# Kernel optimization log

Measured on AMD Instinct MI355X. Metric: run time of the kernel, lower is better.

## Reference

```python
import jax, jax.numpy as jnp
import numpy as np

N, E, F_IN, H, D, C = 50000, 800000, 128, 4, 64, 40
HD = H * D
NEG_SLOPE = 0.2


def setup_inputs() -> dict:
    key = jax.random.key(0)
    ks = jax.random.split(key, 16)
    x = jax.random.normal(ks[0], (N, F_IN), dtype=jnp.float32)
    edge_index = jax.random.randint(ks[1], (2, E), 0, N, dtype=jnp.int64)
    def glorot(k, shape):
        fan = shape[0] + shape[-1]
        return jax.random.normal(k, shape, dtype=jnp.float32) * jnp.sqrt(2.0 / fan)
    params = {
        'W1': glorot(ks[2], (F_IN, HD)), 'as1': glorot(ks[3], (H, D)), 'ad1': glorot(ks[4], (H, D)), 'b1': jnp.zeros((HD,), jnp.float32),
        'W2': glorot(ks[5], (HD, HD)),   'as2': glorot(ks[6], (H, D)), 'ad2': glorot(ks[7], (H, D)), 'b2': jnp.zeros((HD,), jnp.float32),
        'W3': glorot(ks[8], (HD, HD)),   'as3': glorot(ks[9], (H, D)), 'ad3': glorot(ks[10], (H, D)), 'b3': jnp.zeros((HD,), jnp.float32),
        'Wl': glorot(ks[11], (HD, C)),   'bl': jnp.zeros((C,), jnp.float32),
    }
    return {'x': x, 'edge_index': edge_index, **params}


def gat_layer(x, src, dst, W, a_src, a_dst, b):
    # x: [N, F] -> h: [N, H, D]
    h = (x @ W).reshape(N, H, D)
    alpha_s = jnp.sum(h * a_src, axis=-1)  # [N, H]
    alpha_d = jnp.sum(h * a_dst, axis=-1)  # [N, H]
    e = alpha_s[src] + alpha_d[dst]        # [E', H]
    e = jnp.where(e > 0, e, NEG_SLOPE * e)  # leaky_relu
    # segment softmax over destination nodes
    m = jax.ops.segment_max(e, dst, num_segments=N)  # [N, H]
    m = jnp.where(jnp.isfinite(m), m, 0.0)
    ex = jnp.exp(e - m[dst])
    s = jax.ops.segment_sum(ex, dst, num_segments=N)  # [N, H]
    att = ex / (s[dst] + 1e-16)                        # [E', H]
    # weighted scatter-aggregate of source features
    out = jax.ops.segment_sum(h[src] * att[:, :, None], dst, num_segments=N)  # [N, H, D]
    return out.reshape(N, HD) + b


def reference(x, edge_index, W1, as1, ad1, b1, W2, as2, ad2, b2, W3, as3, ad3, b3, Wl, bl):
    # PyG GATConv adds self-loops by default
    loops = jnp.arange(N, dtype=edge_index.dtype)
    src = jnp.concatenate([edge_index[0], loops])
    dst = jnp.concatenate([edge_index[1], loops])
    # dropout is identity in eval mode
    h = jax.nn.elu(gat_layer(x, src, dst, W1, as1, ad1, b1))
    h = jax.nn.elu(gat_layer(h, src, dst, W2, as2, ad2, b2))
    h = jax.nn.elu(gat_layer(h, src, dst, W3, as3, ad3, b3))
    logits = h @ Wl + bl
    return jax.nn.log_softmax(logits, axis=1)
```

## Files before the change

kernel.cpp:

```cpp
#include <hip/hip_runtime.h>
#include <math.h>

#define NN 50000
#define NE 800000
#define ET (NE + NN)
#define FIN 128
#define HDIM 256
#define NHEAD 4
#define NCLS 40
#define NEG 0.2f
#define NB_SCAN ((NN + 255) / 256)

typedef short bf16x8 __attribute__((ext_vector_type(8)));
typedef float f32x4 __attribute__((ext_vector_type(4)));

__device__ __forceinline__ unsigned short f2b(float f) {
    unsigned int u = __float_as_uint(f);
    unsigned int r = (u + 0x7fffu + ((u >> 16) & 1u)) >> 16;
    return (unsigned short)r;
}
__device__ __forceinline__ float b2f(unsigned short u) {
    unsigned int x = ((unsigned int)u) << 16;
    return __uint_as_float(x);
}

__global__ void detect_kernel(const int* __restrict__ ei32, int* __restrict__ flag) {
    int lane = threadIdx.x;
    int nz = ei32[1 + 2 * lane] | ei32[129 + 2 * lane];
    unsigned long long b = __ballot(nz != 0);
    if (lane == 0) *flag = (b == 0ull) ? 1 : 0;
}

__device__ __forceinline__ int load_node(const int* ei32, int is64, long long idx) {
    return is64 ? ei32[2 * idx] : ei32[idx];
}

__global__ void deg_kernel(const int* __restrict__ ei32, const int* __restrict__ flag,
                           int* __restrict__ deg) {
    int e = blockIdx.x * blockDim.x + threadIdx.x;
    if (e >= ET) return;
    int is64 = *flag;
    int d = (e < NE) ? load_node(ei32, is64, (long long)NE + e) : (e - NE);
    atomicAdd(&deg[d], 1);
}

__global__ void scan1(const int* __restrict__ deg, int* __restrict__ incl,
                      int* __restrict__ bsum) {
    __shared__ int sm[256];
    int i = blockIdx.x * 256 + threadIdx.x;
    int v = (i < NN) ? deg[i] : 0;
    sm[threadIdx.x] = v;
    __syncthreads();
    for (int o = 1; o < 256; o <<= 1) {
        int add = (threadIdx.x >= o) ? sm[threadIdx.x - o] : 0;
        __syncthreads();
        sm[threadIdx.x] += add;
        __syncthreads();
    }
    if (i < NN) incl[i] = sm[threadIdx.x];
    if (threadIdx.x == 255) bsum[blockIdx.x] = sm[255];
}

__global__ void scan2(int* __restrict__ bsum) {
    __shared__ int sm[256];
    int t = threadIdx.x;
    sm[t] = (t < NB_SCAN) ? bsum[t] : 0;
    __syncthreads();
    if (t == 0) {
        int run = 0;
        for (int b = 0; b < NB_SCAN; b++) { int v = sm[b]; sm[b] = run; run += v; }
    }
    __syncthreads();
    if (t < NB_SCAN) bsum[t] = sm[t];
}

__global__ void scan3(const int* __restrict__ incl, const int* __restrict__ bsum,
                      const int* __restrict__ deg, int* __restrict__ indptr,
                      int* __restrict__ cursor) {
    int i = blockIdx.x * 256 + threadIdx.x;
    if (i < NN) {
        int v = bsum[blockIdx.x] + incl[i];
        indptr[i + 1] = v;
        cursor[i] = v - deg[i];
    }
    if (i == 0) indptr[0] = 0;
}

__global__ void fill_kernel(const int* __restrict__ ei32, const int* __restrict__ flag,
                            int* __restrict__ cursor, int* __restrict__ esrc) {
    int e = blockIdx.x * blockDim.x + threadIdx.x;
    if (e >= ET) return;
    int is64 = *flag;
    int s, d;
    if (e < NE) {
        s = load_node(ei32, is64, (long long)e);
        d = load_node(ei32, is64, (long long)NE + e);
    } else {
        s = d = e - NE;
    }
    int pos = atomicAdd(&cursor[d], 1);
    esrc[pos] = s;
}

__global__ __launch_bounds__(256) void wconv3_kernel(const float* __restrict__ W1,
                                                     const float* __restrict__ W2,
                                                     const float* __restrict__ W3,
                                                     unsigned short* __restrict__ Wt1,
                                                     unsigned short* __restrict__ Wt2,
                                                     unsigned short* __restrict__ Wt3) {
    __shared__ float sm[32][33];
    int z = blockIdx.z;
    const float* W = (z == 0) ? W1 : (z == 1) ? W2 : W3;
    unsigned short* Wt = (z == 0) ? Wt1 : (z == 1) ? Wt2 : Wt3;
    int K = (z == 0) ? FIN : HDIM;
    int k0 = blockIdx.y * 32;
    if (k0 >= K) return;
    int tx = threadIdx.x & 31, ty = threadIdx.x >> 5;
    int n0 = blockIdx.x * 32;
#pragma unroll
    for (int j = 0; j < 4; j++)
        sm[ty + j * 8][tx] = W[(size_t)(k0 + ty + j * 8) * HDIM + n0 + tx];
    __syncthreads();
#pragma unroll
    for (int j = 0; j < 4; j++)
        Wt[(size_t)(n0 + ty + j * 8) * K + k0 + tx] = f2b(sm[tx][ty + j * 8]);
}

__global__ __launch_bounds__(256) void gemm_mfma(const unsigned short* __restrict__ A,
                                                 const float* __restrict__ A32,
                                                 const unsigned short* __restrict__ Bt,
                                                 unsigned short* __restrict__ Cb,
                                                 const float* __restrict__ a_s,
                                                 const float* __restrict__ a_d,
                                                 float* __restrict__ als,
                                                 float* __restrict__ ald,
                                                 int M, int K) {
    __shared__ unsigned short As[128][72];
    __shared__ unsigned short Bs[64][72];
    int bid = blockIdx.x;
    int xcd = bid & 7, g = bid >> 3;
    int cblk = g & 3, rg = g >> 2;
    int rblk = rg * 8 + xcd;
    int r0 = rblk * 128, n0 = cblk * 64;
    if (r0 >= M) return;

    int t = threadIdx.x;
    int lane = t & 63, wid = t >> 6;

    f32x4 acc[2][4];
#pragma unroll
    for (int m = 0; m < 2; m++)
#pragma unroll
        for (int n = 0; n < 4; n++)
            acc[m][n] = (f32x4){0.f, 0.f, 0.f, 0.f};

    int ar = t >> 1, ah = (t & 1) * 32;
    int arow = r0 + ar; if (arow > M - 1) arow = M - 1;
    const unsigned short* ga = A + (size_t)arow * K + ah;
    const float* ga32 = A32 ? (A32 + (size_t)arow * K + ah) : (const float*)0;
    int bn = t >> 2, bq = (t & 3) * 16;
    const unsigned short* gb = Bt + (size_t)(n0 + bn) * K + bq;

    int fr = lane & 15;
    int kf = (lane >> 4) * 8;

    for (int k0 = 0; k0 < K; k0 += 64) {
        if (A32) {
#pragma unroll
            for (int j = 0; j < 4; j++) {
                float4 fa = *(const float4*)(ga32 + k0 + j * 8);
                float4 fb = *(const float4*)(ga32 + k0 + j * 8 + 4);
                union { ushort4 u[2]; uint4 v; } pk;
                pk.u[0].x = f2b(fa.x); pk.u[0].y = f2b(fa.y);
                pk.u[0].z = f2b(fa.z); pk.u[0].w = f2b(fa.w);
                pk.u[1].x = f2b(fb.x); pk.u[1].y = f2b(fb.y);
                pk.u[1].z = f2b(fb.z); pk.u[1].w = f2b(fb.w);
                *(uint4*)&As[ar][ah + j * 8] = pk.v;
            }
        } else {
#pragma unroll
            for (int j = 0; j < 4; j++)
                *(uint4*)&As[ar][ah + j * 8] = *(const uint4*)(ga + k0 + j * 8);
        }
#pragma unroll
        for (int j = 0; j < 2; j++)
            *(uint4*)&Bs[bn][bq + j * 8] = *(const uint4*)(gb + k0 + j * 8);
        __syncthreads();
#pragma unroll
        for (int kk = 0; kk < 64; kk += 32) {
            bf16x8 a[2], b[4];
#pragma unroll
            for (int m = 0; m < 2; m++)
                a[m] = *(const bf16x8*)&As[wid * 32 + m * 16 + fr][kk + kf];
#pragma unroll
            for (int n = 0; n < 4; n++)
                b[n] = *(const bf16x8*)&Bs[n * 16 + fr][kk + kf];
#pragma unroll
            for (int m = 0; m < 2; m++)
#pragma unroll
                for (int n = 0; n < 4; n++)
                    acc[m][n] = __builtin_amdgcn_mfma_f32_16x16x32_bf16(a[m], b[n], acc[m][n], 0, 0, 0);
        }
        __syncthreads();
    }

    int rbase = r0 + wid * 32 + (lane >> 4) * 4;
    int cbase = n0 + fr;
    int head = n0 >> 6;
    float asv[4], adv[4];
#pragma unroll
    for (int n = 0; n < 4; n++) {
        asv[n] = a_s[cbase + n * 16];
        adv[n] = a_d[cbase + n * 16];
    }
#pragma unroll
    for (int m = 0; m < 2; m++)
#pragma unroll
        for (int q = 0; q < 4; q++) {
            int gr = rbase + m * 16 + q;
            float vs = 0.f, vd = 0.f;
#pragma unroll
            for (int n = 0; n < 4; n++) {
                float v = acc[m][n][q];
                vs += v * asv[n];
                vd += v * adv[n];
            }
#pragma unroll
            for (int o = 8; o > 0; o >>= 1) {
                vs += __shfl_xor(vs, o);
                vd += __shfl_xor(vd, o);
            }
            if (fr == 0 && gr < M) {
                als[gr * NHEAD + head] = vs;
                ald[gr * NHEAD + head] = vd;
            }
        }

    unsigned short (*Cs)[68] = (unsigned short(*)[68])&As[0][0];
    int lr0 = wid * 32 + (lane >> 4) * 4;
#pragma unroll
    for (int m = 0; m < 2; m++)
#pragma unroll
        for (int q = 0; q < 4; q++)
#pragma unroll
            for (int n = 0; n < 4; n++)
                Cs[lr0 + m * 16 + q][fr + n * 16] = f2b(acc[m][n][q]);
    __syncthreads();
    int tr = t >> 4;
    int tc = (t & 15) * 4;
#pragma unroll
    for (int rr = 0; rr < 8; rr++) {
        int lr = tr + rr * 16;
        int gr = r0 + lr;
        if (gr < M) *(ushort4*)(Cb + (size_t)gr * HDIM + n0 + tc) = *(const ushort4*)&Cs[lr][tc];
    }
}

__global__ __launch_bounds__(256) void agg_kernel(const unsigned short* __restrict__ projb,
                                                  const float* __restrict__ als,
                                                  const float* __restrict__ ald,
                                                  const int* __restrict__ indptr,
                                                  const int* __restrict__ esrc,
                                                  const float* __restrict__ bias,
                                                  unsigned short* __restrict__ featb) {
    int wid = threadIdx.x >> 6;
    int v = blockIdx.x * 4 + wid;
    if (v >= NN) return;
    int lane = threadIdx.x & 63;
    int h = lane >> 4;
    int sub = lane & 15;
    int beg = indptr[v], end = indptr[v + 1];
    float adv = ald[v * NHEAD + h];

    float e0 = 0.f, e1 = 0.f;
    int s0r = 0, s1r = 0;
    float m = -INFINITY, ss = 0.f;
    int idx = 0;
    for (int i = beg + sub; i < end; i += 16, idx++) {
        int s = esrc[i];
        float e = als[s * NHEAD + h] + adv;
        e = e > 0.f ? e : NEG * e;
        if (idx == 0) { e0 = e; s0r = s; }
        else if (idx == 1) { e1 = e; s1r = s; }
        if (e > m) {
            ss = ss * __expf(m - e) + 1.f;
            m = e;
        } else {
            ss += __expf(e - m);
        }
    }
#pragma unroll
    for (int o = 8; o > 0; o >>= 1) {
        float m2 = __shfl_xor(m, o);
        float s2 = __shfl_xor(ss, o);
        float mn = fmaxf(m, m2);
        float a = (m == mn) ? ss : ss * __expf(m - mn);
        float b = (m2 == mn) ? s2 : s2 * __expf(m2 - mn);
        m = mn;
        ss = a + b;
    }
    float inv = 1.f / (ss + 1e-16f);

    float4 acc = make_float4(0.f, 0.f, 0.f, 0.f);
    int c = beg;
    int chunk = 0;
    for (; c + 16 <= end; c += 16, chunk++) {
        int sreg;
        float eC;
        if (chunk == 0) { sreg = s0r; eC = e0; }
        else if (chunk == 1) { sreg = s1r; eC = e1; }
        else {
            sreg = esrc[c + sub];
            eC = als[sreg * NHEAD + h] + adv;
            eC = eC > 0.f ? eC : NEG * eC;
        }
        float wreg = __expf(eC - m) * inv;

        ushort4 p[16];
#pragma unroll
        for (int j = 0; j < 16; j++) {
            int s = __shfl(sreg, j);
            p[j] = *(const ushort4*)(projb + (size_t)s * HDIM + (lane << 2));
        }
#pragma unroll
        for (int j = 0; j < 16; j++) {
            float w = __shfl(wreg, (h << 4) | j);
            acc.x += b2f(p[j].x) * w;
            acc.y += b2f(p[j].y) * w;
            acc.z += b2f(p[j].z) * w;
            acc.w += b2f(p[j].w) * w;
        }
    }
    int n = end - c;
    if (n > 0) {
        int sreg;
        float eT;
        if (chunk == 0) { sreg = s0r; eT = e0; }
        else if (chunk == 1) { sreg = s1r; eT = e1; }
        else {
            sreg = (sub < n) ? esrc[c + sub] : 0;
            eT = als[sreg * NHEAD + h] + adv;
            eT = eT > 0.f ? eT : NEG * eT;
        }
        float wreg = (sub < n) ? __expf(eT - m) * inv : 0.f;
        for (int j = 0; j < n; j++) {
            float w = __shfl(wreg, (h << 4) | j);
            int s = __shfl(sreg, j);
            const ushort4 p = *(const ushort4*)(projb + (size_t)s * HDIM + (lane << 2));
            acc.x += b2f(p.x) * w;
            acc.y += b2f(p.y) * w;
            acc.z += b2f(p.z) * w;
            acc.w += b2f(p.w) * w;
        }
    }

    const float4 b4 = *(const float4*)(bias + (lane << 2));
    float4 r;
    r.x = acc.x + b4.x;
    r.y = acc.y + b4.y;
    r.z = acc.z + b4.z;
    r.w = acc.w + b4.w;
    r.x = r.x > 0.f ? r.x : __expf(r.x) - 1.f;
    r.y = r.y > 0.f ? r.y : __expf(r.y) - 1.f;
    r.z = r.z > 0.f ? r.z : __expf(r.z) - 1.f;
    r.w = r.w > 0.f ? r.w : __expf(r.w) - 1.f;
    ushort4 o4;
    o4.x = f2b(r.x); o4.y = f2b(r.y); o4.z = f2b(r.z); o4.w = f2b(r.w);
    *(ushort4*)(featb + (size_t)v * HDIM + (lane << 2)) = o4;
}

__global__ __launch_bounds__(256) void final_kernel(const unsigned short* __restrict__ featb,
                                                    const float* __restrict__ Wl,
                                                    const float* __restrict__ bl,
                                                    float* __restrict__ out) {
    const int BK = 16;
    __shared__ float As[BK][65];
    __shared__ float Bs[BK][65];
    int tx = threadIdx.x & 15, ty = threadIdx.x >> 4;
    int row0 = blockIdx.x * 64;
    float acc[4][4] = {};
    for (int k0 = 0; k0 < HDIM; k0 += BK) {
#pragma unroll
        for (int i = 0; i < 4; i++) {
            int l = threadIdx.x + 256 * i;
            int r = l >> 4, c = l & 15;
            int gr = row0 + r;
            float v = 0.f;
            if (gr < NN) v = b2f(featb[(size_t)gr * HDIM + k0 + c]);
            As[c][r] = v;
        }
#pragma unroll
        for (int i = 0; i < 4; i++) {
            int l = threadIdx.x + 256 * i;
            int r = l >> 6, c = l & 63;
            Bs[r][c] = (c < NCLS) ? Wl[(size_t)(k0 + r) * NCLS + c] : 0.f;
        }
        __syncthreads();
#pragma unroll
        for (int k = 0; k < BK; k++) {
            float a[4], b[4];
#pragma unroll
            for (int i = 0; i < 4; i++) a[i] = As[k][ty + 16 * i];
#pragma unroll
            for (int j = 0; j < 4; j++) b[j] = Bs[k][tx + 16 * j];
#pragma unroll
            for (int i = 0; i < 4; i++)
#pragma unroll
                for (int j = 0; j < 4; j++) acc[i][j] += a[i] * b[j];
        }
        __syncthreads();
    }
    float b0 = bl[tx], b1 = bl[tx + 16], b2 = (tx < 8) ? bl[tx + 32] : 0.f;
#pragma unroll
    for (int i = 0; i < 4; i++) {
        int gr = row0 + ty + 16 * i;
        if (gr >= NN) continue;
        float l0 = acc[i][0] + b0;
        float l1 = acc[i][1] + b1;
        float l2 = (tx < 8) ? acc[i][2] + b2 : -INFINITY;
        float m = fmaxf(fmaxf(l0, l1), l2);
#pragma unroll
        for (int o = 8; o > 0; o >>= 1) m = fmaxf(m, __shfl_xor(m, o));
        float s = __expf(l0 - m) + __expf(l1 - m) + ((tx < 8) ? __expf(l2 - m) : 0.f);
#pragma unroll
        for (int o = 8; o > 0; o >>= 1) s += __shfl_xor(s, o);
        float lse = m + __logf(s);
        out[(size_t)gr * NCLS + tx] = l0 - lse;
        out[(size_t)gr * NCLS + tx + 16] = l1 - lse;
        if (tx < 8) out[(size_t)gr * NCLS + tx + 32] = l2 - lse;
    }
}

extern "C" void kernel_launch(void* const* d_in, const int* in_sizes, int n_in,
                              void* d_out, int out_size, void* d_ws, size_t ws_size,
                              hipStream_t stream) {
    const float* x  = (const float*)d_in[0];
    const int* ei32 = (const int*)d_in[1];
    const float* W1 = (const float*)d_in[2];
    const float* as1 = (const float*)d_in[3];
    const float* ad1 = (const float*)d_in[4];
    const float* b1 = (const float*)d_in[5];
    const float* W2 = (const float*)d_in[6];
    const float* as2 = (const float*)d_in[7];
    const float* ad2 = (const float*)d_in[8];
    const float* b2 = (const float*)d_in[9];
    const float* W3 = (const float*)d_in[10];
    const float* as3 = (const float*)d_in[11];
    const float* ad3 = (const float*)d_in[12];
    const float* b3 = (const float*)d_in[13];
    const float* Wl = (const float*)d_in[14];
    const float* bl = (const float*)d_in[15];
    float* out = (float*)d_out;

    char* w = (char*)d_ws;
    unsigned short* projb = (unsigned short*)w;  w += (size_t)NN * HDIM * 2;
    unsigned short* featb = (unsigned short*)w;  w += (size_t)NN * HDIM * 2;
    unsigned short* Wt1b  = (unsigned short*)w;  w += (size_t)HDIM * FIN * 2;
    unsigned short* Wt2b  = (unsigned short*)w;  w += (size_t)HDIM * HDIM * 2;
    unsigned short* Wt3b  = (unsigned short*)w;  w += (size_t)HDIM * HDIM * 2;
    float* als  = (float*)w;  w += (size_t)NN * NHEAD * 4;
    float* ald  = (float*)w;  w += (size_t)NN * NHEAD * 4;
    int* deg    = (int*)w;    w += (size_t)NN * 4;
    int* incl   = (int*)w;    w += (size_t)NN * 4;
    int* bsum   = (int*)w;    w += 256 * 4;
    int* indptr = (int*)w;    w += (size_t)(NN + 1) * 4;
    int* cursor = (int*)w;    w += (size_t)NN * 4;
    int* esrc   = (int*)w;    w += (size_t)ET * 4;
    int* flag   = (int*)w;    w += 64;

    wconv3_kernel<<<dim3(8, 8, 3), 256, 0, stream>>>(W1, W2, W3, Wt1b, Wt2b, Wt3b);

    hipMemsetAsync(deg, 0, (size_t)NN * 4, stream);
    detect_kernel<<<1, 64, 0, stream>>>(ei32, flag);
    deg_kernel<<<(ET + 255) / 256, 256, 0, stream>>>(ei32, flag, deg);
    scan1<<<NB_SCAN, 256, 0, stream>>>(deg, incl, bsum);
    scan2<<<1, 256, 0, stream>>>(bsum);
    scan3<<<NB_SCAN, 256, 0, stream>>>(incl, bsum, deg, indptr, cursor);
    fill_kernel<<<(ET + 255) / 256, 256, 0, stream>>>(ei32, flag, cursor, esrc);

    int ggrid = 8 * 4 * (((NN + 127) / 128 + 7) / 8);
    int agrid = (NN + 3) / 4;

    gemm_mfma<<<ggrid, 256, 0, stream>>>((const unsigned short*)0, x, Wt1b, projb, as1, ad1, als, ald, NN, FIN);
    agg_kernel<<<agrid, 256, 0, stream>>>(projb, als, ald, indptr, esrc, b1, featb);
    gemm_mfma<<<ggrid, 256, 0, stream>>>(featb, (const float*)0, Wt2b, projb, as2, ad2, als, ald, NN, HDIM);
    agg_kernel<<<agrid, 256, 0, stream>>>(projb, als, ald, indptr, esrc, b2, featb);
    gemm_mfma<<<ggrid, 256, 0, stream>>>(featb, (const float*)0, Wt3b, projb, as3, ad3, als, ald, NN, HDIM);
    agg_kernel<<<agrid, 256, 0, stream>>>(projb, als, ald, indptr, esrc, b3, featb);
    final_kernel<<<(NN + 63) / 64, 256, 0, stream>>>(featb, Wl, bl, out);
}
```

Measured before the change: 435.3 us.

## Prefetch GEMM tiles into registers, pre-convert x to bf16, unify aggregation tail

The GEMM now loads the next K-tile from global memory into registers while the current tile is being computed, a form of software double buffering. The fp32-to-bf16 conversion of x moves out of the first GEMM into a separate conv_kernel using the packed v_cvt_pk_bf16_f32 instruction, which also replaces the manual rounding in the aggregation output store. The aggregation's separate partial-chunk tail loop is folded into the main 16-wide loop by masking weights to zero for missing edges. This trades an extra kernel launch and an extra bf16 copy of x for a simpler GEMM, though the masked tail chunk now issues all 16 gathers even when few edges remain.

```diff
diff --git a/kernel.cpp b/kernel.cpp
--- a/kernel.cpp
+++ b/kernel.cpp
@@ -18,6 +18,11 @@
     unsigned int u = __float_as_uint(f);
     unsigned int r = (u + 0x7fffu + ((u >> 16) & 1u)) >> 16;
     return (unsigned short)r;
+}
+__device__ __forceinline__ unsigned int cvtpk(float lo, float hi) {
+    unsigned int r;
+    asm volatile("v_cvt_pk_bf16_f32 %0, %1, %2" : "=v"(r) : "v"(lo), "v"(hi));
+    return r;
 }
 __device__ __forceinline__ float b2f(unsigned short u) {
     unsigned int x = ((unsigned int)u) << 16;
@@ -100,6 +105,20 @@
     }
     int pos = atomicAdd(&cursor[d], 1);
     esrc[pos] = s;
+}
+
+__global__ __launch_bounds__(256) void conv_kernel(const float* __restrict__ in,
+                                                   unsigned short* __restrict__ out, int n) {
+    int i = (blockIdx.x * 256 + threadIdx.x) * 8;
+    if (i + 8 > n) return;
+    float4 f0 = *(const float4*)(in + i);
+    float4 f1 = *(const float4*)(in + i + 4);
+    uint4 pk;
+    pk.x = cvtpk(f0.x, f0.y);
+    pk.y = cvtpk(f0.z, f0.w);
+    pk.z = cvtpk(f1.x, f1.y);
+    pk.w = cvtpk(f1.z, f1.w);
+    *(uint4*)(out + i) = pk;
 }
 
 __global__ __launch_bounds__(256) void wconv3_kernel(const float* __restrict__ W1,
@@ -127,7 +146,6 @@
 }
 
 __global__ __launch_bounds__(256) void gemm_mfma(const unsigned short* __restrict__ A,
-                                                 const float* __restrict__ A32,
                                                  const unsigned short* __restrict__ Bt,
                                                  unsigned short* __restrict__ Cb,
                                                  const float* __restrict__ a_s,
@@ -157,35 +175,32 @@
     int ar = t >> 1, ah = (t & 1) * 32;
     int arow = r0 + ar; if (arow > M - 1) arow = M - 1;
     const unsigned short* ga = A + (size_t)arow * K + ah;
-    const float* ga32 = A32 ? (A32 + (size_t)arow * K + ah) : (const float*)0;
     int bn = t >> 2, bq = (t & 3) * 16;
     const unsigned short* gb = Bt + (size_t)(n0 + bn) * K + bq;
 
     int fr = lane & 15;
     int kf = (lane >> 4) * 8;
 
+    uint4 ra[4], rb[2], ran[4], rbn[2];
+#pragma unroll
+    for (int j = 0; j < 4; j++) ra[j] = *(const uint4*)(ga + j * 8);
+#pragma unroll
+    for (int j = 0; j < 2; j++) rb[j] = *(const uint4*)(gb + j * 8);
+
     for (int k0 = 0; k0 < K; k0 += 64) {
-        if (A32) {
-#pragma unroll
-            for (int j = 0; j < 4; j++) {
-                float4 fa = *(const float4*)(ga32 + k0 + j * 8);
-                float4 fb = *(const float4*)(ga32 + k0 + j * 8 + 4);
-                union { ushort4 u[2]; uint4 v; } pk;
-                pk.u[0].x = f2b(fa.x); pk.u[0].y = f2b(fa.y);
-                pk.u[0].z = f2b(fa.z); pk.u[0].w = f2b(fa.w);
-                pk.u[1].x = f2b(fb.x); pk.u[1].y = f2b(fb.y);
-                pk.u[1].z = f2b(fb.z); pk.u[1].w = f2b(fb.w);
-                *(uint4*)&As[ar][ah + j * 8] = pk.v;
-            }
-        } else {
-#pragma unroll
-            for (int j = 0; j < 4; j++)
-                *(uint4*)&As[ar][ah + j * 8] = *(const uint4*)(ga + k0 + j * 8);
-        }
+#pragma unroll
+        for (int j = 0; j < 4; j++)
+            *(uint4*)&As[ar][ah + j * 8] = ra[j];
 #pragma unroll
         for (int j = 0; j < 2; j++)
-            *(uint4*)&Bs[bn][bq + j * 8] = *(const uint4*)(gb + k0 + j * 8);
-        __syncthreads();
+            *(uint4*)&Bs[bn][bq + j * 8] = rb[j];
+        __syncthreads();
+        if (k0 + 64 < K) {
+#pragma unroll
+            for (int j = 0; j < 4; j++) ran[j] = *(const uint4*)(ga + k0 + 64 + j * 8);
+#pragma unroll
+            for (int j = 0; j < 2; j++) rbn[j] = *(const uint4*)(gb + k0 + 64 + j * 8);
+        }
 #pragma unroll
         for (int kk = 0; kk < 64; kk += 32) {
             bf16x8 a[2], b[4];
@@ -202,6 +217,10 @@
                     acc[m][n] = __builtin_amdgcn_mfma_f32_16x16x32_bf16(a[m], b[n], acc[m][n], 0, 0, 0);
         }
         __syncthreads();
+#pragma unroll
+        for (int j = 0; j < 4; j++) ra[j] = ran[j];
+#pragma unroll
+        for (int j = 0; j < 2; j++) rb[j] = rbn[j];
     }
 
     int rbase = r0 + wid * 32 + (lane >> 4) * 4;
@@ -302,19 +321,20 @@
     float inv = 1.f / (ss + 1e-16f);
 
     float4 acc = make_float4(0.f, 0.f, 0.f, 0.f);
-    int c = beg;
     int chunk = 0;
-    for (; c + 16 <= end; c += 16, chunk++) {
+    for (int c = beg; c < end; c += 16, chunk++) {
+        int rem = end - c;
         int sreg;
         float eC;
         if (chunk == 0) { sreg = s0r; eC = e0; }
         else if (chunk == 1) { sreg = s1r; eC = e1; }
         else {
-            sreg = esrc[c + sub];
+            int i = c + (sub < rem ? sub : rem - 1);
+            sreg = esrc[i];
             eC = als[sreg * NHEAD + h] + adv;
             eC = eC > 0.f ? eC : NEG * eC;
         }
-        float wreg = __expf(eC - m) * inv;
+        float wreg = (sub < rem) ? __expf(eC - m) * inv : 0.f;
 
         ushort4 p[16];
 #pragma unroll
@@ -329,28 +349,6 @@
             acc.y += b2f(p[j].y) * w;
             acc.z += b2f(p[j].z) * w;
             acc.w += b2f(p[j].w) * w;
-        }
-    }
-    int n = end - c;
-    if (n > 0) {
-        int sreg;
-        float eT;
-        if (chunk == 0) { sreg = s0r; eT = e0; }
-        else if (chunk == 1) { sreg = s1r; eT = e1; }
-        else {
-            sreg = (sub < n) ? esrc[c + sub] : 0;
-            eT = als[sreg * NHEAD + h] + adv;
-            eT = eT > 0.f ? eT : NEG * eT;
-        }
-        float wreg = (sub < n) ? __expf(eT - m) * inv : 0.f;
-        for (int j = 0; j < n; j++) {
-            float w = __shfl(wreg, (h << 4) | j);
-            int s = __shfl(sreg, j);
-            const ushort4 p = *(const ushort4*)(projb + (size_t)s * HDIM + (lane << 2));
-            acc.x += b2f(p.x) * w;
-            acc.y += b2f(p.y) * w;
-            acc.z += b2f(p.z) * w;
-            acc.w += b2f(p.w) * w;
         }
     }
 
@@ -364,9 +362,10 @@
     r.y = r.y > 0.f ? r.y : __expf(r.y) - 1.f;
     r.z = r.z > 0.f ? r.z : __expf(r.z) - 1.f;
     r.w = r.w > 0.f ? r.w : __expf(r.w) - 1.f;
-    ushort4 o4;
-    o4.x = f2b(r.x); o4.y = f2b(r.y); o4.z = f2b(r.z); o4.w = f2b(r.w);
-    *(ushort4*)(featb + (size_t)v * HDIM + (lane << 2)) = o4;
+    uint2 o2;
+    o2.x = cvtpk(r.x, r.y);
+    o2.y = cvtpk(r.z, r.w);
+    *(uint2*)(featb + (size_t)v * HDIM + (lane << 2)) = o2;
 }
 
 __global__ __launch_bounds__(256) void final_kernel(const unsigned short* __restrict__ featb,
@@ -455,6 +454,7 @@
     char* w = (char*)d_ws;
     unsigned short* projb = (unsigned short*)w;  w += (size_t)NN * HDIM * 2;
     unsigned short* featb = (unsigned short*)w;  w += (size_t)NN * HDIM * 2;
+    unsigned short* xb    = (unsigned short*)w;  w += (size_t)NN * FIN * 2;
     unsigned short* Wt1b  = (unsigned short*)w;  w += (size_t)HDIM * FIN * 2;
     unsigned short* Wt2b  = (unsigned short*)w;  w += (size_t)HDIM * HDIM * 2;
     unsigned short* Wt3b  = (unsigned short*)w;  w += (size_t)HDIM * HDIM * 2;
@@ -468,6 +468,7 @@
     int* esrc   = (int*)w;    w += (size_t)ET * 4;
     int* flag   = (int*)w;    w += 64;
 
+    conv_kernel<<<(NN * FIN / 8 + 255) / 256, 256, 0, stream>>>(x, xb, NN * FIN);
     wconv3_kernel<<<dim3(8, 8, 3), 256, 0, stream>>>(W1, W2, W3, Wt1b, Wt2b, Wt3b);
 
     hipMemsetAsync(deg, 0, (size_t)NN * 4, stream);
@@ -481,11 +482,11 @@
     int ggrid = 8 * 4 * (((NN + 127) / 128 + 7) / 8);
     int agrid = (NN + 3) / 4;
 
-    gemm_mfma<<<ggrid, 256, 0, stream>>>((const unsigned short*)0, x, Wt1b, projb, as1, ad1, als, ald, NN, FIN);
+    gemm_mfma<<<ggrid, 256, 0, stream>>>(xb, Wt1b, projb, as1, ad1, als, ald, NN, FIN);
     agg_kernel<<<agrid, 256, 0, stream>>>(projb, als, ald, indptr, esrc, b1, featb);
-    gemm_mfma<<<ggrid, 256, 0, stream>>>(featb, (const float*)0, Wt2b, projb, as2, ad2, als, ald, NN, HDIM);
+    gemm_mfma<<<ggrid, 256, 0, stream>>>(featb, Wt2b, projb, as2, ad2, als, ald, NN, HDIM);
     agg_kernel<<<agrid, 256, 0, stream>>>(projb, als, ald, indptr, esrc, b2, featb);
-    gemm_mfma<<<ggrid, 256, 0, stream>>>(featb, (const float*)0, Wt3b, projb, as3, ad3, als, ald, NN, HDIM);
+    gemm_mfma<<<ggrid, 256, 0, stream>>>(featb, Wt3b, projb, as3, ad3, als, ald, NN, HDIM);
     agg_kernel<<<agrid, 256, 0, stream>>>(projb, als, ald, indptr, esrc, b3, featb);
     final_kernel<<<(NN + 63) / 64, 256, 0, stream>>>(featb, Wl, bl, out);
 }
```

Measured after the change: 597.9 us. 37.4% more time.
